# Optimization experiments

Hardware: AMD Instinct MI355X
Metric: run time of the kernel (lower is better)

Reference implementation:

```python
import jax, jax.numpy as jnp
import numpy as np

K = 16  # neighbors per point (no self-loop)


def _knn_idx(pos, k):
    # pos: (N, 3). Squared euclidean pairwise distances via the ||a-b||^2 expansion.
    n = pos.shape[0]
    sq = jnp.sum(pos * pos, axis=1)                      # (N,)
    d = sq[:, None] + sq[None, :] - 2.0 * (pos @ pos.T)  # (N, N)
    # exclude self (loop=False in torch_cluster.knn_graph)
    diag = jnp.arange(n)
    d = d.at[diag, diag].set(jnp.inf)
    _, idx = jax.lax.top_k(-d, k)                        # k smallest distances -> (N, k)
    return idx


def setup_inputs() -> dict:
    key = jax.random.key(0)
    ks = jax.random.split(key, 6)
    N, C, D = 16384, 64, 64
    x = jax.random.normal(ks[0], (N, C), dtype=jnp.float32)
    pos = jax.random.normal(ks[1], (N, 3), dtype=jnp.float32)
    W1 = jax.random.normal(ks[2], (2 * C, D), dtype=jnp.float32) * 0.08
    b1 = jax.random.normal(ks[3], (D,), dtype=jnp.float32) * 0.02
    W2 = jax.random.normal(ks[4], (D, D), dtype=jnp.float32) * 0.12
    b2 = jax.random.normal(ks[5], (D,), dtype=jnp.float32) * 0.02
    return {"x": x, "pos": pos, "W1": W1, "b1": b1, "W2": W2, "b2": b2}


def reference(x, pos, W1, b1, W2, b2):
    # EdgeConv: for each center i with k-NN neighbors j:
    #   e_ij = MLP([x_i, x_j - x_i]);  out_i = max_j e_ij
    idx = _knn_idx(pos, K)                               # (N, K) int32
    x_j = x[idx]                                         # (N, K, C) gather
    x_i = x[:, None, :]                                  # (N, 1, C)
    ef = jnp.concatenate(
        [jnp.broadcast_to(x_i, x_j.shape), x_j - x_i], axis=-1
    )                                                    # (N, K, 2C)
    h = jax.nn.relu(jnp.einsum("nkc,cd->nkd", ef, W1) + b1)
    h = jnp.einsum("nkd,de->nke", h, W2) + b2            # (N, K, D)
    # each node has exactly K incoming edges -> scatter_max == max over K axis
    return jnp.max(h, axis=1)                            # (N, D)
```

## Files before the change

### kernel.cpp

```cpp
#include <hip/hip_runtime.h>
#include <hip/hip_bf16.h>


#define NPTS 16384
#define CH 64

#define GLO  (-4.5f)
#define GH   0.28125f
#define INVH 3.5555555556f
#define GDIM 32
#define GCELLS (GDIM * GDIM * GDIM)

typedef __attribute__((ext_vector_type(8))) short short8;
typedef __attribute__((ext_vector_type(4))) float floatx4;

__device__ __forceinline__ unsigned short f2bf(float f) {
    unsigned u = __float_as_uint(f);
    u += 0x7FFFu + ((u >> 16) & 1u);
    return (unsigned short)(u >> 16);
}
__device__ __forceinline__ float bf2f(unsigned short u) {
    return __uint_as_float(((unsigned)u) << 16);
}

__device__ __forceinline__ unsigned long long dpp_shr1_u64(unsigned long long x) {
    int lo = (int)(unsigned)(x & 0xFFFFFFFFULL);
    int hi = (int)(unsigned)(x >> 32);
    lo = __builtin_amdgcn_update_dpp(0, lo, 0x111, 0xF, 0xF, false);
    hi = __builtin_amdgcn_update_dpp(0, hi, 0x111, 0xF, 0xF, false);
    return (((unsigned long long)(unsigned)hi) << 32) | (unsigned)lo;
}

__device__ __forceinline__ int cell_of(float x, float y, float z) {
    int cx = (int)floorf((x - GLO) * INVH);
    int cy = (int)floorf((y - GLO) * INVH);
    int cz = (int)floorf((z - GLO) * INVH);
    cx = min(max(cx, 0), GDIM - 1);
    cy = min(max(cy, 0), GDIM - 1);
    cz = min(max(cz, 0), GDIM - 1);
    return (cz * GDIM + cy) * GDIM + cx;
}

__global__ __launch_bounds__(256) void count_prep_kernel(const float* __restrict__ pos,
                                                         int* __restrict__ counts,
                                                         const float* __restrict__ x,
                                                         const float* __restrict__ W1,
                                                         const float* __restrict__ b1,
                                                         float* __restrict__ vout,
                                                         unsigned short* __restrict__ ubuf) {
    __shared__ unsigned short Wct[128 * 72];
    __shared__ unsigned short Abuf[64 * 72];
    __shared__ float Wraw[128 * 64];

    const int t = threadIdx.x;
    if (blockIdx.x < 64) {
        const int i = blockIdx.x * 256 + t;
        atomicAdd(&counts[cell_of(pos[i * 3], pos[i * 3 + 1], pos[i * 3 + 2])], 1);
        return;
    }
    const int bid  = blockIdx.x - 64;
    const int lane = t & 63;
    const int w    = t >> 6;

    {
        const float4* W1v = (const float4*)W1;
        float4* Wr4 = (float4*)Wraw;
#pragma unroll
        for (int i = 0; i < 8; ++i) Wr4[i * 256 + t] = W1v[i * 256 + t];
    }
    __syncthreads();
    {
        const int n = t & 127;
        const int ks = (t >> 7) * 32;
#pragma unroll
        for (int i = 0; i < 32; ++i) {
            const int k = ks + i;
            float val;
            if (n < 64) val = Wraw[k * 64 + n] - Wraw[(64 + k) * 64 + n];
            else        val = Wraw[(64 + k) * 64 + (n - 64)];
            Wct[n * 72 + k] = f2bf(val);
        }
    }
    {
        const int col = t & 63;
#pragma unroll
        for (int i = 0; i < 16; ++i) {
            const int r2 = (t >> 6) + 4 * i;
            const int gp = bid * 64 + r2;
            Abuf[r2 * 72 + col] = f2bf(x[(size_t)gp * CH + col]);
        }
    }
    __syncthreads();

    const int m16 = lane & 15;
    const int q   = lane >> 4;

    floatx4 acc[8];
#pragma unroll
    for (int nt = 0; nt < 8; ++nt) acc[nt] = (floatx4){0.f, 0.f, 0.f, 0.f};

#pragma unroll
    for (int kk = 0; kk < 64; kk += 32) {
        const short8 a = *(const short8*)(Abuf + (w * 16 + m16) * 72 + kk + q * 8);
#pragma unroll
        for (int nt = 0; nt < 8; ++nt) {
            const short8 b = *(const short8*)(Wct + (nt * 16 + m16) * 72 + kk + q * 8);
            acc[nt] = __builtin_amdgcn_mfma_f32_16x16x32_bf16(a, b, acc[nt], 0, 0, 0);
        }
    }

#pragma unroll
    for (int nt = 0; nt < 8; ++nt) {
        const int n = nt * 16 + m16;
#pragma unroll
        for (int r = 0; r < 4; ++r) {
            const int gp = bid * 64 + w * 16 + q * 4 + r;
            if (n < 64) vout[(size_t)gp * CH + n] = acc[nt][r] + b1[n];
            else        ubuf[(size_t)gp * CH + (n - 64)] = f2bf(acc[nt][r]);
        }
    }
}

__global__ __launch_bounds__(1024) void scan_kernel(const int* __restrict__ counts,
                                                    int* __restrict__ starts,
                                                    int* __restrict__ cursor) {
    __shared__ int lds[1024];
    const int t = threadIdx.x;
    int4 v[8];
    const int4* c4 = (const int4*)counts + t * 8;
#pragma unroll
    for (int i = 0; i < 8; ++i) v[i] = c4[i];
    int sum = 0;
#pragma unroll
    for (int i = 0; i < 8; ++i) sum += v[i].x + v[i].y + v[i].z + v[i].w;
    lds[t] = sum;
    __syncthreads();
    for (int off = 1; off < 1024; off <<= 1) {
        int x = 0;
        if (t >= off) x = lds[t - off];
        __syncthreads();
        lds[t] += x;
        __syncthreads();
    }
    int pre = (t == 0) ? 0 : lds[t - 1];
    int4* s4 = (int4*)starts + t * 8;
    int4* u4 = (int4*)cursor + t * 8;
#pragma unroll
    for (int i = 0; i < 8; ++i) {
        int4 o;
        o.x = pre; pre += v[i].x;
        o.y = pre; pre += v[i].y;
        o.z = pre; pre += v[i].z;
        o.w = pre; pre += v[i].w;
        s4[i] = o;
        u4[i] = o;
    }
    if (t == 1023) starts[GCELLS] = pre;
}

__global__ __launch_bounds__(256) void grid_scatter_kernel(const float* __restrict__ pos,
                                                           int* __restrict__ cursor,
                                                           float4* __restrict__ spos,
                                                           unsigned short* __restrict__ sidx) {
    const int i = blockIdx.x * 256 + threadIdx.x;
    const float a = pos[i * 3], b = pos[i * 3 + 1], c = pos[i * 3 + 2];
    const int dst = atomicAdd(&cursor[cell_of(a, b, c)], 1);
    spos[dst] = make_float4(a, b, c, a * a + b * b + c * c);
    sidx[dst] = (unsigned short)i;
}

#define SENT 0xFF800000FFFFFFFFULL
#define NB 4

__global__ __launch_bounds__(64) void knn_grid_kernel(const float* __restrict__ pos,
                                                      const float4* __restrict__ spos,
                                                      const unsigned short* __restrict__ sidx,
                                                      const int* __restrict__ starts,
                                                      unsigned short* __restrict__ knn_out) {
    __shared__ int lds_ex[64];
    __shared__ int lds_st[64];
    const int lane = threadIdx.x;
    const int row  = blockIdx.x;

    const float qx = pos[row * 3 + 0];
    const float qy = pos[row * 3 + 1];
    const float qz = pos[row * 3 + 2];
    const float sqi = qx * qx + qy * qy + qz * qz;
    const int cix = min(max((int)floorf((qx - GLO) * INVH), 0), GDIM - 1);
    const int ciy = min(max((int)floorf((qy - GLO) * INVH), 0), GDIM - 1);
    const int ciz = min(max((int)floorf((qz - GLO) * INVH), 0), GDIM - 1);

    unsigned long long list = SENT;
    float tau = __uint_as_float(0x7F800000u);
    bool first = true;

    int pax = 1, pbx = 0, pay = 1, pby = 0, paz = 1, pbz = 0;

    for (int s = 1; s < GDIM + 1; ++s) {
        const int ax = max(cix - s, 0), bx = min(cix + s, GDIM - 1);
        const int ay = max(ciy - s, 0), by = min(ciy + s, GDIM - 1);
        const int az = max(ciz - s, 0), bz = min(ciz + s, GDIM - 1);
        const int dy = by - ay + 1, dz = bz - az + 1;
        const int npair = dy * dz;
        const float invdy = 1.0f / (float)dy;

        for (int pb = 0; pb < npair; pb += 64) {
            const int pair = pb + lane;
            int stA = 0, lenA = 0, stB = 0, lenB = 0;
            if (pair < npair) {
                const int czo = (int)(((float)pair + 0.5f) * invdy);
                const int cyo = pair - czo * dy;
                const int cy = ay + cyo, cz = az + czo;
                const int rowb = (cz * GDIM + cy) * GDIM;
                const bool inner = cy >= pay && cy <= pby && cz >= paz && cz <= pbz;
                const int bA = inner ? (pax - 1) : bx;
                if (bA >= ax) {
                    stA  = starts[rowb + ax];
                    lenA = starts[rowb + bA + 1] - stA;
                }
                if (inner) {
                    const int aB = pbx + 1;
                    if (bx >= aB) {
                        stB  = starts[rowb + aB];
                        lenB = starts[rowb + bx + 1] - stB;
                    }
                }
            }
#pragma unroll
            for (int setsel = 0; setsel < 2; ++setsel) {
                const int st  = setsel ? stB  : stA;
                const int len = setsel ? lenB : lenA;
                if (__ballot(len > 0) == 0ULL) continue;
                unsigned pfx = (unsigned)len;
#pragma unroll
                for (int off = 1; off < 64; off <<= 1) {
                    const unsigned vv = __shfl_up(pfx, off);
                    if (lane >= off) pfx += vv;
                }
                const int T  = __builtin_amdgcn_readlane((int)pfx, 63);
                lds_ex[lane] = (int)pfx - len;
                lds_st[lane] = st;

                for (int b0 = 0; b0 < T; b0 += 64 * NB) {
                    float4 pts[NB];
                    int    jor[NB];
                    bool   act[NB];
                    bool   live[NB];
#pragma unroll
                    for (int nb = 0; nb < NB; ++nb) {
                        const int bb = b0 + nb * 64;
                        live[nb] = bb < T;
                        act[nb] = false;
                        if (live[nb]) {
                            const int p = bb + lane;
                            int j = 0;
#pragma unroll
                            for (int stp = 32; stp >= 1; stp >>= 1) {
                                const int m = j + stp;
                                if (lds_ex[m] <= p) j = m;
                            }
                            int idx = lds_st[j] + (p - lds_ex[j]);
                            idx = min(idx, NPTS - 1);
                            act[nb] = p < T;
                            pts[nb] = spos[idx];
                            jor[nb] = (int)sidx[idx];
                        }
                    }
#pragma unroll
                    for (int nb = 0; nb < NB; ++nb) {
                        if (!live[nb]) continue;
                        const float dot = fmaf(qx, pts[nb].x,
                                               fmaf(qy, pts[nb].y, qz * pts[nb].z));
                        const float d = fmaf(-2.0f, dot, sqi + pts[nb].w);

                        if (first) {
                            first = false;
                            unsigned kd = __float_as_uint(d);
                            kd = ((int)kd < 0) ? ~kd : (kd | 0x80000000u);
                            unsigned long long key =
                                (((unsigned long long)kd) << 32) | (unsigned)jor[nb];
                            if (!(act[nb] && jor[nb] != row)) key = SENT;
#pragma unroll
                            for (int k = 2; k <= 64; k <<= 1) {
#pragma unroll
                                for (int jj = k >> 1; jj >= 1; jj >>= 1) {
                                    const unsigned long long o = __shfl_xor(key, jj);
                                    const bool takeMin =
                                        (((lane & k) == 0) == ((lane & jj) == 0));
                                    const unsigned long long mn = (key < o) ? key : o;
                                    const unsigned long long mx = (key < o) ? o : key;
                                    key = takeMin ? mn : mx;
                                }
                            }
                            list = key;
                            const unsigned thi = (unsigned)__builtin_amdgcn_readlane(
                                (int)(unsigned)(list >> 32), 15);
                            const unsigned fb =
                                (thi >= 0x80000000u) ? (thi & 0x7FFFFFFFu) : ~thi;
                            tau = __uint_as_float(fb);
                            continue;
                        }

                        const bool cand = act[nb] && (jor[nb] != row) && (d <= tau);
                        unsigned long long mask = __ballot(cand);
                        if (mask) {
                            unsigned kd = __float_as_uint(d);
                            kd = ((int)kd < 0) ? ~kd : (kd | 0x80000000u);
                            do {
                                const int src = __ffsll(mask) - 1;
                                mask &= mask - 1;
                                const unsigned slo =
                                    (unsigned)__builtin_amdgcn_readlane(jor[nb], src);
                                const unsigned shi =
                                    (unsigned)__builtin_amdgcn_readlane((int)kd, src);
                                const unsigned long long v =
                                    (((unsigned long long)shi) << 32) | slo;
                                const unsigned long long prev = dpp_shr1_u64(list);
                                const unsigned long long lr = list;
                                list = (lr < v) ? lr : ((prev < v) ? v : prev);
                            } while (mask);
                            const unsigned thi = (unsigned)__builtin_amdgcn_readlane(
                                (int)(unsigned)(list >> 32), 15);
                            const unsigned fb =
                                (thi >= 0x80000000u) ? (thi & 0x7FFFFFFFu) : ~thi;
                            tau = __uint_as_float(fb);
                        }
                    }
                }
            }
        }

        const float BIG = 1e30f;
        float dout = BIG;
        if (ax > 0)        dout = fminf(dout, qx - (GLO + ax * GH));
        if (bx < GDIM - 1) dout = fminf(dout, (GLO + (bx + 1) * GH) - qx);
        if (ay > 0)        dout = fminf(dout, qy - (GLO + ay * GH));
        if (by < GDIM - 1) dout = fminf(dout, (GLO + (by + 1) * GH) - qy);
        if (az > 0)        dout = fminf(dout, qz - (GLO + az * GH));
        if (bz < GDIM - 1) dout = fminf(dout, (GLO + (bz + 1) * GH) - qz);
        if (dout * dout > tau + 1e-4f) break;
        if (ax == 0 && bx == GDIM - 1 && ay == 0 && by == GDIM - 1 &&
            az == 0 && bz == GDIM - 1) break;
        pax = ax; pbx = bx; pay = ay; pby = by; paz = az; pbz = bz;
    }

    if (lane < 16)
        knn_out[row * 16 + lane] = (unsigned short)(list & 0xFFFFULL);
}

__global__ __launch_bounds__(256) void edge_kernel(const unsigned short* __restrict__ ubuf,
                                                   const float* __restrict__ W2,
                                                   const float* __restrict__ b2,
                                                   const unsigned short* __restrict__ knn,
                                                   float* __restrict__ out) {
    __shared__ unsigned short h[128 * 72];
    __shared__ unsigned short W2t[64 * 72];

    const int t    = threadIdx.x;
    const int lane = t & 63;
    const int w    = t >> 6;

    {
        const int n = t & 63;
        const int kb = (t >> 6) * 16;
#pragma unroll
        for (int i = 0; i < 16; ++i) {
            const int k = kb + i;
            W2t[n * 72 + k] = f2bf(W2[k * 64 + n]);
        }
    }
    {
        const int k = t >> 4;
        const int c = t & 15;
#pragma unroll
        for (int i = 0; i < 8; ++i) {
            const int gn = blockIdx.x * 8 + i;
            const int gj = (int)knn[gn * 16 + k];
            const float4  vv = ((const float4*)(out + (size_t)gn * CH))[c];
            const ushort4 uu = ((const ushort4*)(ubuf + (size_t)gj * CH))[c];
            ushort4 hv;
            hv.x = f2bf(fmaxf(vv.x + bf2f(uu.x), 0.f));
            hv.y = f2bf(fmaxf(vv.y + bf2f(uu.y), 0.f));
            hv.z = f2bf(fmaxf(vv.z + bf2f(uu.z), 0.f));
            hv.w = f2bf(fmaxf(vv.w + bf2f(uu.w), 0.f));
            const int r2 = i * 16 + k;
            *(ushort4*)(h + r2 * 72 + c * 4) = hv;
        }
    }
    __syncthreads();

    const int m16 = lane & 15;
    const int q   = lane >> 4;

    floatx4 acc[2][4];
#pragma unroll
    for (int i = 0; i < 2; ++i)
#pragma unroll
        for (int nt = 0; nt < 4; ++nt) acc[i][nt] = (floatx4){0.f, 0.f, 0.f, 0.f};

#pragma unroll
    for (int kk = 0; kk < 64; kk += 32) {
        const short8 a0 = *(const short8*)(h + ((w * 2 + 0) * 16 + m16) * 72 + kk + q * 8);
        const short8 a1 = *(const short8*)(h + ((w * 2 + 1) * 16 + m16) * 72 + kk + q * 8);
#pragma unroll
        for (int nt = 0; nt < 4; ++nt) {
            const short8 b = *(const short8*)(W2t + (nt * 16 + m16) * 72 + kk + q * 8);
            acc[0][nt] = __builtin_amdgcn_mfma_f32_16x16x32_bf16(a0, b, acc[0][nt], 0, 0, 0);
            acc[1][nt] = __builtin_amdgcn_mfma_f32_16x16x32_bf16(a1, b, acc[1][nt], 0, 0, 0);
        }
    }

#pragma unroll
    for (int i = 0; i < 2; ++i) {
        const int mt = w * 2 + i;
        const int gn = blockIdx.x * 8 + mt;
#pragma unroll
        for (int nt = 0; nt < 4; ++nt) {
            float m0 = fmaxf(fmaxf(acc[i][nt][0], acc[i][nt][1]),
                             fmaxf(acc[i][nt][2], acc[i][nt][3]));
            m0 = fmaxf(m0, __shfl_xor(m0, 16));
            m0 = fmaxf(m0, __shfl_xor(m0, 32));
            if (lane < 16)
                out[(size_t)gn * CH + nt * 16 + lane] = m0 + b2[nt * 16 + lane];
        }
    }
}

extern "C" void kernel_launch(void* const* d_in, const int* in_sizes, int n_in,
                              void* d_out, int out_size, void* d_ws, size_t ws_size,
                              hipStream_t stream) {
    const float* x   = (const float*)d_in[0];
    const float* pos = (const float*)d_in[1];
    const float* W1  = (const float*)d_in[2];
    const float* b1  = (const float*)d_in[3];
    const float* W2  = (const float*)d_in[4];
    const float* b2  = (const float*)d_in[5];
    float* out = (float*)d_out;

    char* ws = (char*)d_ws;
    unsigned short* knn  = (unsigned short*)ws;
    unsigned short* ubuf = (unsigned short*)(ws + 524288);
    int*    counts = (int*)(ws + 2621440);
    int*    starts = (int*)(ws + 2752512);
    int*    cursor = (int*)(ws + 2883600);
    float4* spos   = (float4*)(ws + 3014672);
    unsigned short* sidx = (unsigned short*)(ws + 3276816);

    hipMemsetAsync(counts, 0, GCELLS * sizeof(int), stream);
    count_prep_kernel<<<320, 256, 0, stream>>>(pos, counts, x, W1, b1, out, ubuf);
    scan_kernel<<<1, 1024, 0, stream>>>(counts, starts, cursor);
    grid_scatter_kernel<<<NPTS / 256, 256, 0, stream>>>(pos, cursor, spos, sidx);
    knn_grid_kernel<<<NPTS, 64, 0, stream>>>(pos, spos, sidx, starts, knn);
    edge_kernel<<<NPTS / 8, 256, 0, stream>>>(ubuf, W2, b2, knn, out);
}
```

Measured before the change: 144.8 us.

## Fuse all stages into one persistent cooperative kernel with grid syncs

Replaces the memset and five separate kernel launches with a single cooperative persistent kernel that uses grid.sync between stages: zeroing counts, the W1 projection, counting, scan, scatter, kNN search and the edge MLP. The kNN stage now processes queries in grid-sorted order via an atomic work counter, four queries per wave, which improves spatial locality. The edge stage also uses dynamic tile fetching. The aim is to remove launch gaps and improve cache locality, at the cost of grid-wide barriers, a single-block scan and lower occupancy limits.

```diff
diff --git a/kernel.cpp b/kernel.cpp
--- a/kernel.cpp
+++ b/kernel.cpp
@@ -1,15 +1,20 @@
 #include <hip/hip_runtime.h>
 #include <hip/hip_bf16.h>
+#include <hip/hip_cooperative_groups.h>
+
+namespace cg = cooperative_groups;
 
 
 #define NPTS 16384
 #define CH 64
-
 #define GLO  (-4.5f)
 #define GH   0.28125f
 #define INVH 3.5555555556f
 #define GDIM 32
 #define GCELLS (GDIM * GDIM * GDIM)
+#define NTILES (NPTS / 8)
+#define SENT 0xFF800000FFFFFFFFULL
+#define NB 4
 
 typedef __attribute__((ext_vector_type(8))) short short8;
 typedef __attribute__((ext_vector_type(4))) float floatx4;
@@ -22,7 +27,6 @@
 __device__ __forceinline__ float bf2f(unsigned short u) {
     return __uint_as_float(((unsigned)u) << 16);
 }
-
 __device__ __forceinline__ unsigned long long dpp_shr1_u64(unsigned long long x) {
     int lo = (int)(unsigned)(x & 0xFFFFFFFFULL);
     int hi = (int)(unsigned)(x >> 32);
@@ -30,7 +34,15 @@
     hi = __builtin_amdgcn_update_dpp(0, hi, 0x111, 0xF, 0xF, false);
     return (((unsigned long long)(unsigned)hi) << 32) | (unsigned)lo;
 }
-
+__device__ __forceinline__ unsigned wave_iscan(unsigned x) {
+    x += (unsigned)__builtin_amdgcn_update_dpp(0, (int)x, 0x111, 0xF, 0xF, true);
+    x += (unsigned)__builtin_amdgcn_update_dpp(0, (int)x, 0x112, 0xF, 0xF, true);
+    x += (unsigned)__builtin_amdgcn_update_dpp(0, (int)x, 0x114, 0xF, 0xF, true);
+    x += (unsigned)__builtin_amdgcn_update_dpp(0, (int)x, 0x118, 0xF, 0xF, true);
+    x += (unsigned)__builtin_amdgcn_update_dpp(0, (int)x, 0x142, 0xA, 0xF, true);
+    x += (unsigned)__builtin_amdgcn_update_dpp(0, (int)x, 0x143, 0xC, 0xF, true);
+    return x;
+}
 __device__ __forceinline__ int cell_of(float x, float y, float z) {
     int cx = (int)floorf((x - GLO) * INVH);
     int cy = (int)floorf((y - GLO) * INVH);
@@ -41,387 +53,383 @@
     return (cz * GDIM + cy) * GDIM + cx;
 }
 
-__global__ __launch_bounds__(256) void count_prep_kernel(const float* __restrict__ pos,
-                                                         int* __restrict__ counts,
-                                                         const float* __restrict__ x,
-                                                         const float* __restrict__ W1,
-                                                         const float* __restrict__ b1,
-                                                         float* __restrict__ vout,
-                                                         unsigned short* __restrict__ ubuf) {
-    __shared__ unsigned short Wct[128 * 72];
-    __shared__ unsigned short Abuf[64 * 72];
-    __shared__ float Wraw[128 * 64];
-
-    const int t = threadIdx.x;
-    if (blockIdx.x < 64) {
-        const int i = blockIdx.x * 256 + t;
+#define SMEM_BYTES 27664
+
+__global__ __launch_bounds__(256, 4) void mega_kernel(
+        const float* __restrict__ pos, const float* __restrict__ x,
+        const float* __restrict__ W1, const float* __restrict__ b1,
+        const float* __restrict__ W2, const float* __restrict__ b2,
+        float* __restrict__ out, int* __restrict__ counts,
+        int* __restrict__ starts, int* __restrict__ cursor,
+        float4* __restrict__ spos, unsigned short* __restrict__ sidx,
+        unsigned short* __restrict__ knn, unsigned short* __restrict__ ubuf,
+        int* __restrict__ ctrs) {
+    __shared__ alignas(16) char smem[SMEM_BYTES];
+    cg::grid_group grid = cg::this_grid();
+
+    const int t     = threadIdx.x;
+    const int lane  = t & 63;
+    const int w     = t >> 6;
+    const int gsize = gridDim.x * 256;
+    const int gtid  = blockIdx.x * 256 + t;
+
+    for (int c = gtid; c < GCELLS; c += gsize) counts[c] = 0;
+    if (gtid == 0) { ctrs[0] = 0; ctrs[1] = 0; }
+
+    {
+        unsigned short* Wct  = (unsigned short*)smem;
+        unsigned short* Abuf = (unsigned short*)(smem + 18432);
+        const int m16 = lane & 15;
+        const int q   = lane >> 4;
+        if (blockIdx.x < NPTS / 64) {
+            {
+                const int n  = t & 127;
+                const int ks = (t >> 7) * 32;
+#pragma unroll
+                for (int i = 0; i < 32; ++i) {
+                    const int k = ks + i;
+                    float val;
+                    if (n < 64) val = W1[k * 64 + n] - W1[(64 + k) * 64 + n];
+                    else        val = W1[(64 + k) * 64 + (n - 64)];
+                    Wct[n * 72 + k] = f2bf(val);
+                }
+            }
+            for (int tile = blockIdx.x; tile < NPTS / 64; tile += gridDim.x) {
+                __syncthreads();
+                {
+                    const int col = t & 63;
+#pragma unroll
+                    for (int i = 0; i < 16; ++i) {
+                        const int r2 = (t >> 6) + 4 * i;
+                        const int gp = tile * 64 + r2;
+                        Abuf[r2 * 72 + col] = f2bf(x[(size_t)gp * CH + col]);
+                    }
+                }
+                __syncthreads();
+                floatx4 acc[8];
+#pragma unroll
+                for (int nt = 0; nt < 8; ++nt) acc[nt] = (floatx4){0.f, 0.f, 0.f, 0.f};
+#pragma unroll
+                for (int kk = 0; kk < 64; kk += 32) {
+                    const short8 a = *(const short8*)(Abuf + (w * 16 + m16) * 72 + kk + q * 8);
+#pragma unroll
+                    for (int nt = 0; nt < 8; ++nt) {
+                        const short8 b = *(const short8*)(Wct + (nt * 16 + m16) * 72 + kk + q * 8);
+                        acc[nt] = __builtin_amdgcn_mfma_f32_16x16x32_bf16(a, b, acc[nt], 0, 0, 0);
+                    }
+                }
+#pragma unroll
+                for (int nt = 0; nt < 8; ++nt) {
+                    const int n = nt * 16 + m16;
+#pragma unroll
+                    for (int r = 0; r < 4; ++r) {
+                        const int gp = tile * 64 + w * 16 + q * 4 + r;
+                        if (n < 64) out[(size_t)gp * CH + n] = acc[nt][r] + b1[n];
+                        else        ubuf[(size_t)gp * CH + (n - 64)] = f2bf(acc[nt][r]);
+                    }
+                }
+            }
+        }
+    }
+    grid.sync();
+
+    for (int i = gtid; i < NPTS; i += gsize)
         atomicAdd(&counts[cell_of(pos[i * 3], pos[i * 3 + 1], pos[i * 3 + 2])], 1);
-        return;
+    grid.sync();
+
+    if (blockIdx.x == 0) {
+        int* slds = (int*)smem;
+        const int4* c4 = (const int4*)counts + t * 32;
+        int sum = 0;
+#pragma unroll 8
+        for (int i = 0; i < 32; ++i) {
+            const int4 u = c4[i];
+            sum += u.x + u.y + u.z + u.w;
+        }
+        slds[t] = sum;
+        __syncthreads();
+        for (int off = 1; off < 256; off <<= 1) {
+            int vv = 0;
+            if (t >= off) vv = slds[t - off];
+            __syncthreads();
+            slds[t] += vv;
+            __syncthreads();
+        }
+        int pre = (t == 0) ? 0 : slds[t - 1];
+        int4* s4 = (int4*)starts + t * 32;
+        int4* u4 = (int4*)cursor + t * 32;
+#pragma unroll 8
+        for (int i = 0; i < 32; ++i) {
+            const int4 u = c4[i];
+            int4 o;
+            o.x = pre; pre += u.x;
+            o.y = pre; pre += u.y;
+            o.z = pre; pre += u.z;
+            o.w = pre; pre += u.w;
+            s4[i] = o;
+            u4[i] = o;
+        }
+        if (t == 255) starts[GCELLS] = pre;
     }
-    const int bid  = blockIdx.x - 64;
-    const int lane = t & 63;
-    const int w    = t >> 6;
+    grid.sync();
+
+    for (int i = gtid; i < NPTS; i += gsize) {
+        const float a = pos[i * 3], b = pos[i * 3 + 1], c = pos[i * 3 + 2];
+        const int dst = atomicAdd(&cursor[cell_of(a, b, c)], 1);
+        spos[dst] = make_float4(a, b, c, a * a + b * b + c * c);
+        sidx[dst] = (unsigned short)i;
+    }
+    grid.sync();
 
     {
-        const float4* W1v = (const float4*)W1;
-        float4* Wr4 = (float4*)Wraw;
-#pragma unroll
-        for (int i = 0; i < 8; ++i) Wr4[i * 256 + t] = W1v[i * 256 + t];
-    }
-    __syncthreads();
-    {
-        const int n = t & 127;
-        const int ks = (t >> 7) * 32;
-#pragma unroll
-        for (int i = 0; i < 32; ++i) {
-            const int k = ks + i;
-            float val;
-            if (n < 64) val = Wraw[k * 64 + n] - Wraw[(64 + k) * 64 + n];
-            else        val = Wraw[(64 + k) * 64 + (n - 64)];
-            Wct[n * 72 + k] = f2bf(val);
-        }
-    }
-    {
-        const int col = t & 63;
-#pragma unroll
-        for (int i = 0; i < 16; ++i) {
-            const int r2 = (t >> 6) + 4 * i;
-            const int gp = bid * 64 + r2;
-            Abuf[r2 * 72 + col] = f2bf(x[(size_t)gp * CH + col]);
-        }
-    }
-    __syncthreads();
-
-    const int m16 = lane & 15;
-    const int q   = lane >> 4;
-
-    floatx4 acc[8];
-#pragma unroll
-    for (int nt = 0; nt < 8; ++nt) acc[nt] = (floatx4){0.f, 0.f, 0.f, 0.f};
-
-#pragma unroll
-    for (int kk = 0; kk < 64; kk += 32) {
-        const short8 a = *(const short8*)(Abuf + (w * 16 + m16) * 72 + kk + q * 8);
-#pragma unroll
-        for (int nt = 0; nt < 8; ++nt) {
-            const short8 b = *(const short8*)(Wct + (nt * 16 + m16) * 72 + kk + q * 8);
-            acc[nt] = __builtin_amdgcn_mfma_f32_16x16x32_bf16(a, b, acc[nt], 0, 0, 0);
-        }
-    }
-
-#pragma unroll
-    for (int nt = 0; nt < 8; ++nt) {
-        const int n = nt * 16 + m16;
-#pragma unroll
-        for (int r = 0; r < 4; ++r) {
-            const int gp = bid * 64 + w * 16 + q * 4 + r;
-            if (n < 64) vout[(size_t)gp * CH + n] = acc[nt][r] + b1[n];
-            else        ubuf[(size_t)gp * CH + (n - 64)] = f2bf(acc[nt][r]);
-        }
-    }
-}
-
-__global__ __launch_bounds__(1024) void scan_kernel(const int* __restrict__ counts,
-                                                    int* __restrict__ starts,
-                                                    int* __restrict__ cursor) {
-    __shared__ int lds[1024];
-    const int t = threadIdx.x;
-    int4 v[8];
-    const int4* c4 = (const int4*)counts + t * 8;
-#pragma unroll
-    for (int i = 0; i < 8; ++i) v[i] = c4[i];
-    int sum = 0;
-#pragma unroll
-    for (int i = 0; i < 8; ++i) sum += v[i].x + v[i].y + v[i].z + v[i].w;
-    lds[t] = sum;
-    __syncthreads();
-    for (int off = 1; off < 1024; off <<= 1) {
-        int x = 0;
-        if (t >= off) x = lds[t - off];
-        __syncthreads();
-        lds[t] += x;
-        __syncthreads();
-    }
-    int pre = (t == 0) ? 0 : lds[t - 1];
-    int4* s4 = (int4*)starts + t * 8;
-    int4* u4 = (int4*)cursor + t * 8;
-#pragma unroll
-    for (int i = 0; i < 8; ++i) {
-        int4 o;
-        o.x = pre; pre += v[i].x;
-        o.y = pre; pre += v[i].y;
-        o.z = pre; pre += v[i].z;
-        o.w = pre; pre += v[i].w;
-        s4[i] = o;
-        u4[i] = o;
-    }
-    if (t == 1023) starts[GCELLS] = pre;
-}
-
-__global__ __launch_bounds__(256) void grid_scatter_kernel(const float* __restrict__ pos,
-                                                           int* __restrict__ cursor,
-                                                           float4* __restrict__ spos,
-                                                           unsigned short* __restrict__ sidx) {
-    const int i = blockIdx.x * 256 + threadIdx.x;
-    const float a = pos[i * 3], b = pos[i * 3 + 1], c = pos[i * 3 + 2];
-    const int dst = atomicAdd(&cursor[cell_of(a, b, c)], 1);
-    spos[dst] = make_float4(a, b, c, a * a + b * b + c * c);
-    sidx[dst] = (unsigned short)i;
-}
-
-#define SENT 0xFF800000FFFFFFFFULL
-#define NB 4
-
-__global__ __launch_bounds__(64) void knn_grid_kernel(const float* __restrict__ pos,
-                                                      const float4* __restrict__ spos,
-                                                      const unsigned short* __restrict__ sidx,
-                                                      const int* __restrict__ starts,
-                                                      unsigned short* __restrict__ knn_out) {
-    __shared__ int lds_ex[64];
-    __shared__ int lds_st[64];
-    const int lane = threadIdx.x;
-    const int row  = blockIdx.x;
-
-    const float qx = pos[row * 3 + 0];
-    const float qy = pos[row * 3 + 1];
-    const float qz = pos[row * 3 + 2];
-    const float sqi = qx * qx + qy * qy + qz * qz;
-    const int cix = min(max((int)floorf((qx - GLO) * INVH), 0), GDIM - 1);
-    const int ciy = min(max((int)floorf((qy - GLO) * INVH), 0), GDIM - 1);
-    const int ciz = min(max((int)floorf((qz - GLO) * INVH), 0), GDIM - 1);
-
-    unsigned long long list = SENT;
-    float tau = __uint_as_float(0x7F800000u);
-    bool first = true;
-
-    int pax = 1, pbx = 0, pay = 1, pby = 0, paz = 1, pbz = 0;
-
-    for (int s = 1; s < GDIM + 1; ++s) {
-        const int ax = max(cix - s, 0), bx = min(cix + s, GDIM - 1);
-        const int ay = max(ciy - s, 0), by = min(ciy + s, GDIM - 1);
-        const int az = max(ciz - s, 0), bz = min(ciz + s, GDIM - 1);
-        const int dy = by - ay + 1, dz = bz - az + 1;
-        const int npair = dy * dz;
-        const float invdy = 1.0f / (float)dy;
-
-        for (int pb = 0; pb < npair; pb += 64) {
-            const int pair = pb + lane;
-            int stA = 0, lenA = 0, stB = 0, lenB = 0;
-            if (pair < npair) {
-                const int czo = (int)(((float)pair + 0.5f) * invdy);
-                const int cyo = pair - czo * dy;
-                const int cy = ay + cyo, cz = az + czo;
-                const int rowb = (cz * GDIM + cy) * GDIM;
-                const bool inner = cy >= pay && cy <= pby && cz >= paz && cz <= pbz;
-                const int bA = inner ? (pax - 1) : bx;
-                if (bA >= ax) {
-                    stA  = starts[rowb + ax];
-                    lenA = starts[rowb + bA + 1] - stA;
-                }
-                if (inner) {
-                    const int aB = pbx + 1;
-                    if (bx >= aB) {
-                        stB  = starts[rowb + aB];
-                        lenB = starts[rowb + bx + 1] - stB;
-                    }
-                }
-            }
-#pragma unroll
-            for (int setsel = 0; setsel < 2; ++setsel) {
-                const int st  = setsel ? stB  : stA;
-                const int len = setsel ? lenB : lenA;
-                if (__ballot(len > 0) == 0ULL) continue;
-                unsigned pfx = (unsigned)len;
-#pragma unroll
-                for (int off = 1; off < 64; off <<= 1) {
-                    const unsigned vv = __shfl_up(pfx, off);
-                    if (lane >= off) pfx += vv;
-                }
-                const int T  = __builtin_amdgcn_readlane((int)pfx, 63);
-                lds_ex[lane] = (int)pfx - len;
-                lds_st[lane] = st;
-
-                for (int b0 = 0; b0 < T; b0 += 64 * NB) {
-                    float4 pts[NB];
-                    int    jor[NB];
-                    bool   act[NB];
-                    bool   live[NB];
-#pragma unroll
-                    for (int nb = 0; nb < NB; ++nb) {
-                        const int bb = b0 + nb * 64;
-                        live[nb] = bb < T;
-                        act[nb] = false;
-                        if (live[nb]) {
-                            const int p = bb + lane;
-                            int j = 0;
-#pragma unroll
-                            for (int stp = 32; stp >= 1; stp >>= 1) {
-                                const int m = j + stp;
-                                if (lds_ex[m] <= p) j = m;
+        int* lds_ex = (int*)smem + w * 64;
+        int* lds_st = (int*)(smem + 1024) + w * 64;
+        while (true) {
+            int sq0 = 0;
+            if (lane == 0) sq0 = atomicAdd(&ctrs[0], 4);
+            sq0 = __shfl(sq0, 0);
+            if (sq0 >= NPTS) break;
+            for (int qi = 0; qi < 4; ++qi) {
+                const int sq = sq0 + qi;
+                const float4 qv = spos[sq];
+                const float qx = qv.x, qy = qv.y, qz = qv.z, sqi = qv.w;
+                const int qrow = (int)sidx[sq];
+                const int cix = min(max((int)floorf((qx - GLO) * INVH), 0), GDIM - 1);
+                const int ciy = min(max((int)floorf((qy - GLO) * INVH), 0), GDIM - 1);
+                const int ciz = min(max((int)floorf((qz - GLO) * INVH), 0), GDIM - 1);
+
+                unsigned long long list = SENT;
+                float tau = __uint_as_float(0x7F800000u);
+                bool first = true;
+                int pax = 1, pbx = 0, pay = 1, pby = 0, paz = 1, pbz = 0;
+
+                for (int s = 1; s < GDIM + 1; ++s) {
+                    const int ax = max(cix - s, 0), bx = min(cix + s, GDIM - 1);
+                    const int ay = max(ciy - s, 0), by = min(ciy + s, GDIM - 1);
+                    const int az = max(ciz - s, 0), bz = min(ciz + s, GDIM - 1);
+                    const int dy = by - ay + 1, dz = bz - az + 1;
+                    const int npair = dy * dz;
+                    const float invdy = 1.0f / (float)dy;
+
+                    for (int pb = 0; pb < npair; pb += 64) {
+                        const int pair = pb + lane;
+                        int stA = 0, lenA = 0, stB = 0, lenB = 0;
+                        if (pair < npair) {
+                            const int czo = (int)(((float)pair + 0.5f) * invdy);
+                            const int cyo = pair - czo * dy;
+                            const int cy = ay + cyo, cz = az + czo;
+                            const int rowb = (cz * GDIM + cy) * GDIM;
+                            const bool inner = cy >= pay && cy <= pby &&
+                                               cz >= paz && cz <= pbz;
+                            const int bA = inner ? (pax - 1) : bx;
+                            if (bA >= ax) {
+                                stA  = starts[rowb + ax];
+                                lenA = starts[rowb + bA + 1] - stA;
                             }
-                            int idx = lds_st[j] + (p - lds_ex[j]);
-                            idx = min(idx, NPTS - 1);
-                            act[nb] = p < T;
-                            pts[nb] = spos[idx];
-                            jor[nb] = (int)sidx[idx];
+                            if (inner) {
+                                const int aB = pbx + 1;
+                                if (bx >= aB) {
+                                    stB  = starts[rowb + aB];
+                                    lenB = starts[rowb + bx + 1] - stB;
+                                }
+                            }
+                        }
+#pragma unroll
+                        for (int setsel = 0; setsel < 2; ++setsel) {
+                            const int st  = setsel ? stB  : stA;
+                            const int len = setsel ? lenB : lenA;
+                            if (__ballot(len > 0) == 0ULL) continue;
+                            const unsigned pfx = wave_iscan((unsigned)len);
+                            const int T  = __builtin_amdgcn_readlane((int)pfx, 63);
+                            lds_ex[lane] = (int)pfx - len;
+                            lds_st[lane] = st;
+
+                            for (int b0 = 0; b0 < T; b0 += 64 * NB) {
+                                float4 pts[NB];
+                                int    jor[NB];
+                                bool   act[NB];
+                                bool   live[NB];
+#pragma unroll
+                                for (int nb = 0; nb < NB; ++nb) {
+                                    const int bb = b0 + nb * 64;
+                                    live[nb] = bb < T;
+                                    act[nb] = false;
+                                    if (live[nb]) {
+                                        const int p = bb + lane;
+                                        int j = 0;
+#pragma unroll
+                                        for (int stp = 32; stp >= 1; stp >>= 1) {
+                                            const int m = j + stp;
+                                            if (lds_ex[m] <= p) j = m;
+                                        }
+                                        int idx = lds_st[j] + (p - lds_ex[j]);
+                                        idx = min(idx, NPTS - 1);
+                                        act[nb] = p < T;
+                                        pts[nb] = spos[idx];
+                                        jor[nb] = (int)sidx[idx];
+                                    }
+                                }
+#pragma unroll
+                                for (int nb = 0; nb < NB; ++nb) {
+                                    if (!live[nb]) continue;
+                                    const float dot = fmaf(qx, pts[nb].x,
+                                                     fmaf(qy, pts[nb].y, qz * pts[nb].z));
+                                    const float d = fmaf(-2.0f, dot, sqi + pts[nb].w);
+
+                                    if (first) {
+                                        first = false;
+                                        unsigned kd = __float_as_uint(d);
+                                        kd = ((int)kd < 0) ? ~kd : (kd | 0x80000000u);
+                                        unsigned long long key =
+                                            (((unsigned long long)kd) << 32) |
+                                            (unsigned)jor[nb];
+                                        if (!(act[nb] && jor[nb] != qrow)) key = SENT;
+#pragma unroll
+                                        for (int k = 2; k <= 64; k <<= 1) {
+#pragma unroll
+                                            for (int jj = k >> 1; jj >= 1; jj >>= 1) {
+                                                const unsigned long long o =
+                                                    __shfl_xor(key, jj);
+                                                const bool takeMin =
+                                                    (((lane & k) == 0) == ((lane & jj) == 0));
+                                                const unsigned long long mn = (key < o) ? key : o;
+                                                const unsigned long long mx = (key < o) ? o : key;
+                                                key = takeMin ? mn : mx;
+                                            }
+                                        }
+                                        list = key;
+                                        const unsigned thi = (unsigned)
+                                            __builtin_amdgcn_readlane(
+                                                (int)(unsigned)(list >> 32), 15);
+                                        const unsigned fb = (thi >= 0x80000000u)
+                                            ? (thi & 0x7FFFFFFFu) : ~thi;
+                                        tau = __uint_as_float(fb);
+                                        continue;
+                                    }
+
+                                    const bool cand = act[nb] && (jor[nb] != qrow) &&
+                                                      (d <= tau);
+                                    unsigned long long mask = __ballot(cand);
+                                    if (mask) {
+                                        unsigned kd = __float_as_uint(d);
+                                        kd = ((int)kd < 0) ? ~kd : (kd | 0x80000000u);
+                                        do {
+                                            const int src = __ffsll(mask) - 1;
+                                            mask &= mask - 1;
+                                            const unsigned slo = (unsigned)
+                                                __builtin_amdgcn_readlane(jor[nb], src);
+                                            const unsigned shi = (unsigned)
+                                                __builtin_amdgcn_readlane((int)kd, src);
+                                            const unsigned long long v =
+                                                (((unsigned long long)shi) << 32) | slo;
+                                            const unsigned long long prev = dpp_shr1_u64(list);
+                                            const unsigned long long lr = list;
+                                            list = (lr < v) ? lr : ((prev < v) ? v : prev);
+                                        } while (mask);
+                                        const unsigned thi = (unsigned)
+                                            __builtin_amdgcn_readlane(
+                                                (int)(unsigned)(list >> 32), 15);
+                                        const unsigned fb = (thi >= 0x80000000u)
+                                            ? (thi & 0x7FFFFFFFu) : ~thi;
+                                        tau = __uint_as_float(fb);
+                                    }
+                                }
+                            }
                         }
                     }
-#pragma unroll
-                    for (int nb = 0; nb < NB; ++nb) {
-                        if (!live[nb]) continue;
-                        const float dot = fmaf(qx, pts[nb].x,
-                                               fmaf(qy, pts[nb].y, qz * pts[nb].z));
-                        const float d = fmaf(-2.0f, dot, sqi + pts[nb].w);
-
-                        if (first) {
-                            first = false;
-                            unsigned kd = __float_as_uint(d);
-                            kd = ((int)kd < 0) ? ~kd : (kd | 0x80000000u);
-                            unsigned long long key =
-                                (((unsigned long long)kd) << 32) | (unsigned)jor[nb];
-                            if (!(act[nb] && jor[nb] != row)) key = SENT;
-#pragma unroll
-                            for (int k = 2; k <= 64; k <<= 1) {
-#pragma unroll
-                                for (int jj = k >> 1; jj >= 1; jj >>= 1) {
-                                    const unsigned long long o = __shfl_xor(key, jj);
-                                    const bool takeMin =
-                                        (((lane & k) == 0) == ((lane & jj) == 0));
-                                    const unsigned long long mn = (key < o) ? key : o;
-                                    const unsigned long long mx = (key < o) ? o : key;
-                                    key = takeMin ? mn : mx;
-                                }
-                            }
-                            list = key;
-                            const unsigned thi = (unsigned)__builtin_amdgcn_readlane(
-                                (int)(unsigned)(list >> 32), 15);
-                            const unsigned fb =
-                                (thi >= 0x80000000u) ? (thi & 0x7FFFFFFFu) : ~thi;
-                            tau = __uint_as_float(fb);
-                            continue;
-                        }
-
-                        const bool cand = act[nb] && (jor[nb] != row) && (d <= tau);
-                        unsigned long long mask = __ballot(cand);
-                        if (mask) {
-                            unsigned kd = __float_as_uint(d);
-                            kd = ((int)kd < 0) ? ~kd : (kd | 0x80000000u);
-                            do {
-                                const int src = __ffsll(mask) - 1;
-                                mask &= mask - 1;
-                                const unsigned slo =
-                                    (unsigned)__builtin_amdgcn_readlane(jor[nb], src);
-                                const unsigned shi =
-                                    (unsigned)__builtin_amdgcn_readlane((int)kd, src);
-                                const unsigned long long v =
-                                    (((unsigned long long)shi) << 32) | slo;
-                                const unsigned long long prev = dpp_shr1_u64(list);
-                                const unsigned long long lr = list;
-                                list = (lr < v) ? lr : ((prev < v) ? v : prev);
-                            } while (mask);
-                            const unsigned thi = (unsigned)__builtin_amdgcn_readlane(
-                                (int)(unsigned)(list >> 32), 15);
-                            const unsigned fb =
-                                (thi >= 0x80000000u) ? (thi & 0x7FFFFFFFu) : ~thi;
-                            tau = __uint_as_float(fb);
-                        }
-                    }
-                }
-            }
-        }
-
-        const float BIG = 1e30f;
-        float dout = BIG;
-        if (ax > 0)        dout = fminf(dout, qx - (GLO + ax * GH));
-        if (bx < GDIM - 1) dout = fminf(dout, (GLO + (bx + 1) * GH) - qx);
-        if (ay > 0)        dout = fminf(dout, qy - (GLO + ay * GH));
-        if (by < GDIM - 1) dout = fminf(dout, (GLO + (by + 1) * GH) - qy);
-        if (az > 0)        dout = fminf(dout, qz - (GLO + az * GH));
-        if (bz < GDIM - 1) dout = fminf(dout, (GLO + (bz + 1) * GH) - qz);
-        if (dout * dout > tau + 1e-4f) break;
-        if (ax == 0 && bx == GDIM - 1 && ay == 0 && by == GDIM - 1 &&
-            az == 0 && bz == GDIM - 1) break;
-        pax = ax; pbx = bx; pay = ay; pby = by; paz = az; pbz = bz;
+
+                    const float BIG = 1e30f;
+                    float dout = BIG;
+                    if (ax > 0)        dout = fminf(dout, qx - (GLO + ax * GH));
+                    if (bx < GDIM - 1) dout = fminf(dout, (GLO + (bx + 1) * GH) - qx);
+                    if (ay > 0)        dout = fminf(dout, qy - (GLO + ay * GH));
+                    if (by < GDIM - 1) dout = fminf(dout, (GLO + (by + 1) * GH) - qy);
+                    if (az > 0)        dout = fminf(dout, qz - (GLO + az * GH));
+                    if (bz < GDIM - 1) dout = fminf(dout, (GLO + (bz + 1) * GH) - qz);
+                    if (dout * dout > tau + 1e-4f) break;
+                    if (ax == 0 && bx == GDIM - 1 && ay == 0 && by == GDIM - 1 &&
+                        az == 0 && bz == GDIM - 1) break;
+                    pax = ax; pbx = bx; pay = ay; pby = by; paz = az; pbz = bz;
+                }
+
+                if (lane < 16)
+                    knn[qrow * 16 + lane] = (unsigned short)(list & 0xFFFFULL);
+            }
+        }
     }
-
-    if (lane < 16)
-        knn_out[row * 16 + lane] = (unsigned short)(list & 0xFFFFULL);
-}
-
-__global__ __launch_bounds__(256) void edge_kernel(const unsigned short* __restrict__ ubuf,
-                                                   const float* __restrict__ W2,
-                                                   const float* __restrict__ b2,
-                                                   const unsigned short* __restrict__ knn,
-                                                   float* __restrict__ out) {
-    __shared__ unsigned short h[128 * 72];
-    __shared__ unsigned short W2t[64 * 72];
-
-    const int t    = threadIdx.x;
-    const int lane = t & 63;
-    const int w    = t >> 6;
+    grid.sync();
 
     {
-        const int n = t & 63;
-        const int kb = (t >> 6) * 16;
-#pragma unroll
-        for (int i = 0; i < 16; ++i) {
-            const int k = kb + i;
-            W2t[n * 72 + k] = f2bf(W2[k * 64 + n]);
-        }
-    }
-    {
-        const int k = t >> 4;
-        const int c = t & 15;
-#pragma unroll
-        for (int i = 0; i < 8; ++i) {
-            const int gn = blockIdx.x * 8 + i;
-            const int gj = (int)knn[gn * 16 + k];
-            const float4  vv = ((const float4*)(out + (size_t)gn * CH))[c];
-            const ushort4 uu = ((const ushort4*)(ubuf + (size_t)gj * CH))[c];
-            ushort4 hv;
-            hv.x = f2bf(fmaxf(vv.x + bf2f(uu.x), 0.f));
-            hv.y = f2bf(fmaxf(vv.y + bf2f(uu.y), 0.f));
-            hv.z = f2bf(fmaxf(vv.z + bf2f(uu.z), 0.f));
-            hv.w = f2bf(fmaxf(vv.w + bf2f(uu.w), 0.f));
-            const int r2 = i * 16 + k;
-            *(ushort4*)(h + r2 * 72 + c * 4) = hv;
-        }
-    }
-    __syncthreads();
-
-    const int m16 = lane & 15;
-    const int q   = lane >> 4;
-
-    floatx4 acc[2][4];
-#pragma unroll
-    for (int i = 0; i < 2; ++i)
-#pragma unroll
-        for (int nt = 0; nt < 4; ++nt) acc[i][nt] = (floatx4){0.f, 0.f, 0.f, 0.f};
-
-#pragma unroll
-    for (int kk = 0; kk < 64; kk += 32) {
-        const short8 a0 = *(const short8*)(h + ((w * 2 + 0) * 16 + m16) * 72 + kk + q * 8);
-        const short8 a1 = *(const short8*)(h + ((w * 2 + 1) * 16 + m16) * 72 + kk + q * 8);
-#pragma unroll
-        for (int nt = 0; nt < 4; ++nt) {
-            const short8 b = *(const short8*)(W2t + (nt * 16 + m16) * 72 + kk + q * 8);
-            acc[0][nt] = __builtin_amdgcn_mfma_f32_16x16x32_bf16(a0, b, acc[0][nt], 0, 0, 0);
-            acc[1][nt] = __builtin_amdgcn_mfma_f32_16x16x32_bf16(a1, b, acc[1][nt], 0, 0, 0);
-        }
-    }
-
-#pragma unroll
-    for (int i = 0; i < 2; ++i) {
-        const int mt = w * 2 + i;
-        const int gn = blockIdx.x * 8 + mt;
-#pragma unroll
-        for (int nt = 0; nt < 4; ++nt) {
-            float m0 = fmaxf(fmaxf(acc[i][nt][0], acc[i][nt][1]),
-                             fmaxf(acc[i][nt][2], acc[i][nt][3]));
-            m0 = fmaxf(m0, __shfl_xor(m0, 16));
-            m0 = fmaxf(m0, __shfl_xor(m0, 32));
-            if (lane < 16)
-                out[(size_t)gn * CH + nt * 16 + lane] = m0 + b2[nt * 16 + lane];
+        unsigned short* h   = (unsigned short*)smem;
+        unsigned short* W2t = (unsigned short*)(smem + 18432);
+        int* sm_tile = (int*)(smem + 27648);
+        const int m16 = lane & 15;
+        const int q   = lane >> 4;
+        {
+            const int n = t & 63;
+            const int kb = (t >> 6) * 16;
+#pragma unroll
+            for (int i = 0; i < 16; ++i) {
+                const int k = kb + i;
+                W2t[n * 72 + k] = f2bf(W2[k * 64 + n]);
+            }
+        }
+        __syncthreads();
+        while (true) {
+            if (t == 0) *sm_tile = atomicAdd(&ctrs[1], 1);
+            __syncthreads();
+            const int tile = *sm_tile;
+            if (tile >= NTILES) break;
+            {
+                const int k = t >> 4;
+                const int c = t & 15;
+#pragma unroll
+                for (int i = 0; i < 8; ++i) {
+                    const int gn = tile * 8 + i;
+                    const int gj = (int)knn[gn * 16 + k];
+                    const float4  vv = ((const float4*)(out + (size_t)gn * CH))[c];
+                    const ushort4 uu = ((const ushort4*)(ubuf + (size_t)gj * CH))[c];
+                    ushort4 hv;
+                    hv.x = f2bf(fmaxf(vv.x + bf2f(uu.x), 0.f));
+                    hv.y = f2bf(fmaxf(vv.y + bf2f(uu.y), 0.f));
+                    hv.z = f2bf(fmaxf(vv.z + bf2f(uu.z), 0.f));
+                    hv.w = f2bf(fmaxf(vv.w + bf2f(uu.w), 0.f));
+                    const int r2 = i * 16 + k;
+                    *(ushort4*)(h + r2 * 72 + c * 4) = hv;
+                }
+            }
+            __syncthreads();
+            floatx4 acc[2][4];
+#pragma unroll
+            for (int i = 0; i < 2; ++i)
+#pragma unroll
+                for (int nt = 0; nt < 4; ++nt) acc[i][nt] = (floatx4){0.f, 0.f, 0.f, 0.f};
+#pragma unroll
+            for (int kk = 0; kk < 64; kk += 32) {
+                const short8 a0 = *(const short8*)(h + ((w * 2 + 0) * 16 + m16) * 72 + kk + q * 8);
+                const short8 a1 = *(const short8*)(h + ((w * 2 + 1) * 16 + m16) * 72 + kk + q * 8);
+#pragma unroll
+                for (int nt = 0; nt < 4; ++nt) {
+                    const short8 b = *(const short8*)(W2t + (nt * 16 + m16) * 72 + kk + q * 8);
+                    acc[0][nt] = __builtin_amdgcn_mfma_f32_16x16x32_bf16(a0, b, acc[0][nt], 0, 0, 0);
+                    acc[1][nt] = __builtin_amdgcn_mfma_f32_16x16x32_bf16(a1, b, acc[1][nt], 0, 0, 0);
+                }
+            }
+#pragma unroll
+            for (int i = 0; i < 2; ++i) {
+                const int mt = w * 2 + i;
+                const int gn = tile * 8 + mt;
+#pragma unroll
+                for (int nt = 0; nt < 4; ++nt) {
+                    float m0 = fmaxf(fmaxf(acc[i][nt][0], acc[i][nt][1]),
+                                     fmaxf(acc[i][nt][2], acc[i][nt][3]));
+                    m0 = fmaxf(m0, __shfl_xor(m0, 16));
+                    m0 = fmaxf(m0, __shfl_xor(m0, 32));
+                    if (lane < 16)
+                        out[(size_t)gn * CH + nt * 16 + lane] = m0 + b2[nt * 16 + lane];
+                }
+            }
+            __syncthreads();
         }
     }
 }
@@ -445,11 +453,18 @@
     int*    cursor = (int*)(ws + 2883600);
     float4* spos   = (float4*)(ws + 3014672);
     unsigned short* sidx = (unsigned short*)(ws + 3276816);
-
-    hipMemsetAsync(counts, 0, GCELLS * sizeof(int), stream);
-    count_prep_kernel<<<320, 256, 0, stream>>>(pos, counts, x, W1, b1, out, ubuf);
-    scan_kernel<<<1, 1024, 0, stream>>>(counts, starts, cursor);
-    grid_scatter_kernel<<<NPTS / 256, 256, 0, stream>>>(pos, cursor, spos, sidx);
-    knn_grid_kernel<<<NPTS, 64, 0, stream>>>(pos, spos, sidx, starts, knn);
-    edge_kernel<<<NPTS / 8, 256, 0, stream>>>(ubuf, W2, b2, knn, out);
-}
+    int*    ctrs   = (int*)(ws + 3309584);
+
+    int occ = 0;
+    hipOccupancyMaxActiveBlocksPerMultiprocessor(&occ, mega_kernel, 256, 0);
+    if (occ < 1) occ = 1;
+    int gridN = occ * 256;
+    if (gridN > 2048) gridN = 2048;
+
+    void* args[] = {(void*)&pos, (void*)&x, (void*)&W1, (void*)&b1,
+                    (void*)&W2, (void*)&b2, (void*)&out, (void*)&counts,
+                    (void*)&starts, (void*)&cursor, (void*)&spos, (void*)&sidx,
+                    (void*)&knn, (void*)&ubuf, (void*)&ctrs};
+    hipLaunchCooperativeKernel((const void*)mega_kernel, dim3(gridN), dim3(256),
+                               args, 0, stream);
+}
```

New measurement: 513.3 us. 254% more time.

## Batch kNN candidate insertion via LDS buffer and bitonic merge; iterate queries in cell order

Applied to the files above, without the earlier changes.

Replaces the serial per-candidate insertion into the wave-distributed top-16 list with buffering of candidates in LDS and a periodic flush. The flush bitonic-sorts up to 64 candidates and merges them with the current list. Blocks now process queries in grid-sorted order, which improves locality of neighbour-cell reads, and the prefix scan uses DPP row ops instead of shuffles. The trade-off is a staler tau threshold between flushes, so more candidates get admitted, plus the fixed cost of each sort network.

```diff
diff --git a/kernel.cpp b/kernel.cpp
--- a/kernel.cpp
+++ b/kernel.cpp
@@ -22,15 +22,15 @@
 __device__ __forceinline__ float bf2f(unsigned short u) {
     return __uint_as_float(((unsigned)u) << 16);
 }
-
-__device__ __forceinline__ unsigned long long dpp_shr1_u64(unsigned long long x) {
-    int lo = (int)(unsigned)(x & 0xFFFFFFFFULL);
-    int hi = (int)(unsigned)(x >> 32);
-    lo = __builtin_amdgcn_update_dpp(0, lo, 0x111, 0xF, 0xF, false);
-    hi = __builtin_amdgcn_update_dpp(0, hi, 0x111, 0xF, 0xF, false);
-    return (((unsigned long long)(unsigned)hi) << 32) | (unsigned)lo;
-}
-
+__device__ __forceinline__ unsigned wave_iscan(unsigned x) {
+    x += (unsigned)__builtin_amdgcn_update_dpp(0, (int)x, 0x111, 0xF, 0xF, true);
+    x += (unsigned)__builtin_amdgcn_update_dpp(0, (int)x, 0x112, 0xF, 0xF, true);
+    x += (unsigned)__builtin_amdgcn_update_dpp(0, (int)x, 0x114, 0xF, 0xF, true);
+    x += (unsigned)__builtin_amdgcn_update_dpp(0, (int)x, 0x118, 0xF, 0xF, true);
+    x += (unsigned)__builtin_amdgcn_update_dpp(0, (int)x, 0x142, 0xA, 0xF, true);
+    x += (unsigned)__builtin_amdgcn_update_dpp(0, (int)x, 0x143, 0xC, 0xF, true);
+    return x;
+}
 __device__ __forceinline__ int cell_of(float x, float y, float z) {
     int cx = (int)floorf((x - GLO) * INVH);
     int cy = (int)floorf((y - GLO) * INVH);
@@ -172,20 +172,19 @@
 #define SENT 0xFF800000FFFFFFFFULL
 #define NB 4
 
-__global__ __launch_bounds__(64) void knn_grid_kernel(const float* __restrict__ pos,
-                                                      const float4* __restrict__ spos,
+__global__ __launch_bounds__(64) void knn_grid_kernel(const float4* __restrict__ spos,
                                                       const unsigned short* __restrict__ sidx,
                                                       const int* __restrict__ starts,
                                                       unsigned short* __restrict__ knn_out) {
     __shared__ int lds_ex[64];
     __shared__ int lds_st[64];
+    __shared__ unsigned long long buf[64];
     const int lane = threadIdx.x;
-    const int row  = blockIdx.x;
-
-    const float qx = pos[row * 3 + 0];
-    const float qy = pos[row * 3 + 1];
-    const float qz = pos[row * 3 + 2];
-    const float sqi = qx * qx + qy * qy + qz * qz;
+    const int sq   = blockIdx.x;
+
+    const float4 qv = spos[sq];
+    const float qx = qv.x, qy = qv.y, qz = qv.z, sqi = qv.w;
+    const int qrow = (int)sidx[sq];
     const int cix = min(max((int)floorf((qx - GLO) * INVH), 0), GDIM - 1);
     const int ciy = min(max((int)floorf((qy - GLO) * INVH), 0), GDIM - 1);
     const int ciz = min(max((int)floorf((qz - GLO) * INVH), 0), GDIM - 1);
@@ -193,6 +192,39 @@
     unsigned long long list = SENT;
     float tau = __uint_as_float(0x7F800000u);
     bool first = true;
+    int nbuf = 0;
+
+    auto do_flush = [&]() {
+        unsigned long long ck = (lane < nbuf) ? buf[lane] : SENT;
+#pragma unroll
+        for (int k = 2; k <= 64; k <<= 1) {
+#pragma unroll
+            for (int jj = k >> 1; jj >= 1; jj >>= 1) {
+                const unsigned long long o = __shfl_xor(ck, jj);
+                const bool takeMin = (((lane & k) == 0) == ((lane & jj) == 0));
+                const unsigned long long mn = (ck < o) ? ck : o;
+                const unsigned long long mx = (ck < o) ? o : ck;
+                ck = takeMin ? mn : mx;
+            }
+        }
+        const unsigned long long cv = __shfl(ck, 31 - lane);
+        unsigned long long m = SENT;
+        if (lane < 16) m = list;
+        else if (lane < 32) m = cv;
+#pragma unroll
+        for (int jj = 16; jj >= 1; jj >>= 1) {
+            const unsigned long long o = __shfl_xor(m, jj);
+            const unsigned long long mn = (m < o) ? m : o;
+            const unsigned long long mx = (m < o) ? o : m;
+            m = ((lane & jj) == 0) ? mn : mx;
+        }
+        list = m;
+        const unsigned thi = (unsigned)__builtin_amdgcn_readlane(
+            (int)(unsigned)(list >> 32), 15);
+        const unsigned fb = (thi >= 0x80000000u) ? (thi & 0x7FFFFFFFu) : ~thi;
+        tau = __uint_as_float(fb);
+        nbuf = 0;
+    };
 
     int pax = 1, pbx = 0, pay = 1, pby = 0, paz = 1, pbz = 0;
 
@@ -231,13 +263,8 @@
                 const int st  = setsel ? stB  : stA;
                 const int len = setsel ? lenB : lenA;
                 if (__ballot(len > 0) == 0ULL) continue;
-                unsigned pfx = (unsigned)len;
-#pragma unroll
-                for (int off = 1; off < 64; off <<= 1) {
-                    const unsigned vv = __shfl_up(pfx, off);
-                    if (lane >= off) pfx += vv;
-                }
-                const int T  = __builtin_amdgcn_readlane((int)pfx, 63);
+                const unsigned pfx = wave_iscan((unsigned)len);
+                const int T = __builtin_amdgcn_readlane((int)pfx, 63);
                 lds_ex[lane] = (int)pfx - len;
                 lds_st[lane] = st;
 
@@ -279,7 +306,7 @@
                             kd = ((int)kd < 0) ? ~kd : (kd | 0x80000000u);
                             unsigned long long key =
                                 (((unsigned long long)kd) << 32) | (unsigned)jor[nb];
-                            if (!(act[nb] && jor[nb] != row)) key = SENT;
+                            if (!(act[nb] && jor[nb] != qrow)) key = SENT;
 #pragma unroll
                             for (int k = 2; k <= 64; k <<= 1) {
 #pragma unroll
@@ -301,34 +328,28 @@
                             continue;
                         }
 
-                        const bool cand = act[nb] && (jor[nb] != row) && (d <= tau);
-                        unsigned long long mask = __ballot(cand);
+                        const bool cand = act[nb] && (jor[nb] != qrow) && (d <= tau);
+                        const unsigned long long mask = __ballot(cand);
                         if (mask) {
-                            unsigned kd = __float_as_uint(d);
-                            kd = ((int)kd < 0) ? ~kd : (kd | 0x80000000u);
-                            do {
-                                const int src = __ffsll(mask) - 1;
-                                mask &= mask - 1;
-                                const unsigned slo =
-                                    (unsigned)__builtin_amdgcn_readlane(jor[nb], src);
-                                const unsigned shi =
-                                    (unsigned)__builtin_amdgcn_readlane((int)kd, src);
-                                const unsigned long long v =
-                                    (((unsigned long long)shi) << 32) | slo;
-                                const unsigned long long prev = dpp_shr1_u64(list);
-                                const unsigned long long lr = list;
-                                list = (lr < v) ? lr : ((prev < v) ? v : prev);
-                            } while (mask);
-                            const unsigned thi = (unsigned)__builtin_amdgcn_readlane(
-                                (int)(unsigned)(list >> 32), 15);
-                            const unsigned fb =
-                                (thi >= 0x80000000u) ? (thi & 0x7FFFFFFFu) : ~thi;
-                            tau = __uint_as_float(fb);
+                            const int cnt = __popcll(mask);
+                            if (nbuf + cnt > 64) do_flush();
+                            if (cand) {
+                                unsigned kd = __float_as_uint(d);
+                                kd = ((int)kd < 0) ? ~kd : (kd | 0x80000000u);
+                                const unsigned long long key =
+                                    (((unsigned long long)kd) << 32) | (unsigned)jor[nb];
+                                const int rank =
+                                    __popcll(mask & ((1ULL << lane) - 1ULL));
+                                buf[nbuf + rank] = key;
+                            }
+                            nbuf += cnt;
                         }
                     }
                 }
             }
         }
+
+        if (nbuf) do_flush();
 
         const float BIG = 1e30f;
         float dout = BIG;
@@ -345,7 +366,7 @@
     }
 
     if (lane < 16)
-        knn_out[row * 16 + lane] = (unsigned short)(list & 0xFFFFULL);
+        knn_out[qrow * 16 + lane] = (unsigned short)(list & 0xFFFFULL);
 }
 
 __global__ __launch_bounds__(256) void edge_kernel(const unsigned short* __restrict__ ubuf,
@@ -450,6 +471,6 @@
     count_prep_kernel<<<320, 256, 0, stream>>>(pos, counts, x, W1, b1, out, ubuf);
     scan_kernel<<<1, 1024, 0, stream>>>(counts, starts, cursor);
     grid_scatter_kernel<<<NPTS / 256, 256, 0, stream>>>(pos, cursor, spos, sidx);
-    knn_grid_kernel<<<NPTS, 64, 0, stream>>>(pos, spos, sidx, starts, knn);
+    knn_grid_kernel<<<NPTS, 64, 0, stream>>>(spos, sidx, starts, knn);
     edge_kernel<<<NPTS / 8, 256, 0, stream>>>(ubuf, W2, b2, knn, out);
 }
```

Result: slower. 151.2 us (+4.4%).
